# Kernel optimization log

Measured on AMD Instinct MI355X. Metric: run time of the kernel, lower is better.

Reference implementation:

```python
import jax, jax.numpy as jnp
import numpy as np

INS, OUTS = 768, 64
B, S = 8, 2048


def setup_inputs() -> dict:
    key = jax.random.key(0)
    ks = jax.random.split(key, 7)
    scale = 1.0 / np.sqrt(INS)
    inputs = jax.random.normal(ks[0], (B, S, INS), dtype=jnp.float32)
    Wq = jax.random.uniform(ks[1], (INS, OUTS), jnp.float32, -scale, scale)
    bq = jax.random.uniform(ks[2], (OUTS,), jnp.float32, -scale, scale)
    Wk = jax.random.uniform(ks[3], (INS, OUTS), jnp.float32, -scale, scale)
    bk = jax.random.uniform(ks[4], (OUTS,), jnp.float32, -scale, scale)
    Wv = jax.random.uniform(ks[5], (INS, OUTS), jnp.float32, -scale, scale)
    bv = jax.random.uniform(ks[6], (OUTS,), jnp.float32, -scale, scale)
    return {"inputs": inputs, "Wq": Wq, "bq": bq, "Wk": Wk, "bk": bk, "Wv": Wv, "bv": bv}


def reference(inputs, Wq, bq, Wk, bk, Wv, bv):
    # QKV projections: [B, S, ins] @ [ins, outs] -> [B, S, outs]
    q = jnp.einsum('bsi,io->bso', inputs, Wq) + bq
    k = jnp.einsum('bsi,io->bso', inputs, Wk) + bk
    v = jnp.einsum('bsi,io->bso', inputs, Wv) + bv
    dim_k = k.shape[-1]
    # scores: [B, S, S] (materialized, as in the original bmm-based impl)
    att = jnp.einsum('bqd,bkd->bqk', q, k) / jnp.sqrt(jnp.asarray(dim_k, q.dtype))
    att_soft = jax.nn.softmax(att, axis=-1)
    out = jnp.einsum('bqk,bkd->bqd', att_soft, v)
    return out
```

## Files before the change

### kernel.cpp

```cpp
#include <hip/hip_runtime.h>
#include <hip/hip_bf16.h>
#include <stdint.h>

#define INS 768
#define OUTS 64
#define BB 8
#define SS 2048
#define LDP 40

typedef __attribute__((ext_vector_type(8))) short short8;
typedef __attribute__((ext_vector_type(4))) float f32x4;

__device__ inline unsigned short f2bf(float f) {
  union { float f; uint32_t u; } v; v.f = f;
  uint32_t r = v.u + 0x7FFFu + ((v.u >> 16) & 1u);
  return (unsigned short)(r >> 16);
}

__device__ inline short8 cvt8hw(float4 a, float4 b) {
  union { __hip_bfloat162 h[4]; short8 s; } u;
  u.h[0] = __float22bfloat162_rn(make_float2(a.x, a.y));
  u.h[1] = __float22bfloat162_rn(make_float2(a.z, a.w));
  u.h[2] = __float22bfloat162_rn(make_float2(b.x, b.y));
  u.h[3] = __float22bfloat162_rn(make_float2(b.z, b.w));
  return u.s;
}
__device__ inline short8 cvt8w(const float* wf, float scl) {
  union { __hip_bfloat162 h[4]; short8 s; } u;
#pragma unroll
  for (int j = 0; j < 4; ++j)
    u.h[j] = __float22bfloat162_rn(make_float2(wf[2 * j] * scl, wf[2 * j + 1] * scl));
  return u.s;
}

__global__ __launch_bounds__(512) void qkv(
    const float* __restrict__ X,
    const float* __restrict__ Wq, const float* __restrict__ bq,
    const float* __restrict__ Wk, const float* __restrict__ bk,
    const float* __restrict__ Wv, const float* __restrict__ bv,
    unsigned short* __restrict__ Qg, unsigned short* __restrict__ Kg,
    unsigned short* __restrict__ Vtg) {
  __shared__ float Cbuf[4][64][13];
  const int tid  = threadIdx.x;
  const int wave = tid >> 6, lane = tid & 63;
  const int chg  = wave & 3, kh = wave >> 2;
  const int quad = lane >> 4, l16 = lane & 15;
  const int row0 = blockIdx.x * 16;
  const float* Xr = X + (size_t)(row0 + l16) * INS + kh * 384 + quad * 8;

  const float* Wm[3]; const float* Bm[3]; float scl[3]; int col0[3];
#pragma unroll
  for (int nt = 0; nt < 3; ++nt) {
    const int n0 = chg * 48 + nt * 16;
    const int mat = n0 >> 6;
    col0[nt] = n0 & 63;
    if (mat == 0)      { Wm[nt] = Wq; Bm[nt] = bq; scl[nt] = 0.125f; }
    else if (mat == 1) { Wm[nt] = Wk; Bm[nt] = bk; scl[nt] = 1.0f; }
    else               { Wm[nt] = Wv; Bm[nt] = bv; scl[nt] = 1.0f; }
  }

  f32x4 acc[3];
#pragma unroll
  for (int i = 0; i < 3; ++i) acc[i] = (f32x4){0.f, 0.f, 0.f, 0.f};

#pragma unroll 2
  for (int kc = 0; kc < 12; ++kc) {
    const int ko = kc * 32;
    const int kk = kh * 384 + ko;
    float4 x0 = *reinterpret_cast<const float4*>(Xr + ko);
    float4 x1 = *reinterpret_cast<const float4*>(Xr + ko + 4);
    float wf[3][8];
#pragma unroll
    for (int nt = 0; nt < 3; ++nt) {
      const float* src = Wm[nt] + (size_t)(kk + quad * 8) * OUTS + col0[nt] + l16;
#pragma unroll
      for (int j = 0; j < 8; ++j) wf[nt][j] = src[(size_t)j * OUTS];
    }
    short8 a = cvt8hw(x0, x1);
#pragma unroll
    for (int nt = 0; nt < 3; ++nt) {
      short8 b = cvt8w(wf[nt], scl[nt]);
      acc[nt] = __builtin_amdgcn_mfma_f32_16x16x32_bf16(a, b, acc[nt], 0, 0, 0);
    }
  }

  if (kh == 1) {
#pragma unroll
    for (int nt = 0; nt < 3; ++nt)
#pragma unroll
      for (int r = 0; r < 4; ++r) Cbuf[chg][lane][nt * 4 + r] = acc[nt][r];
  }
  __syncthreads();
  if (kh == 0) {
#pragma unroll
    for (int nt = 0; nt < 3; ++nt)
#pragma unroll
      for (int r = 0; r < 4; ++r) acc[nt][r] += Cbuf[chg][lane][nt * 4 + r];

    const int gm0 = row0 + quad * 4;
#pragma unroll
    for (int nt = 0; nt < 3; ++nt) {
      const int n = chg * 48 + nt * 16 + l16;
      const float bias = Bm[nt][col0[nt] + l16] * scl[nt];
      if (n < 128) {
        unsigned short* dstbase = (n < 64) ? Qg : Kg;
        const int nn = n & 63;
#pragma unroll
        for (int r = 0; r < 4; ++r)
          dstbase[(size_t)(gm0 + r) * OUTS + nn] = f2bf(acc[nt][r] + bias);
      } else {
        const int d = n - 128;
        const int batch = gm0 >> 11, s0 = gm0 & 2047;
        ushort4 pk;
        pk.x = f2bf(acc[nt][0] + bias);
        pk.y = f2bf(acc[nt][1] + bias);
        pk.z = f2bf(acc[nt][2] + bias);
        pk.w = f2bf(acc[nt][3] + bias);
        *reinterpret_cast<ushort4*>(&Vtg[((size_t)batch * OUTS + d) * SS + s0]) = pk;
      }
    }
  }
}

__global__ __launch_bounds__(256) void attn(
    const unsigned short* __restrict__ Qg, const unsigned short* __restrict__ Kg,
    const unsigned short* __restrict__ Vtg,
    float* __restrict__ OP, float* __restrict__ LS) {
  __shared__ __align__(16) unsigned short Ps[4][2][16 * LDP];
  const int tid  = threadIdx.x;
  const int wave = tid >> 6, lane = tid & 63;
  const int quad = lane >> 4, l16 = lane & 15;
  const int bt  = blockIdx.x >> 6;
  const int rem = blockIdx.x & 63;
  const int qb  = rem >> 2, ksl = rem & 3;
  const int q0 = qb * 128 + wave * 32;
  const unsigned short* Qb = Qg + (size_t)bt * SS * OUTS;
  const unsigned short* Kb = Kg + (size_t)bt * SS * OUTS;
  const unsigned short* Vb = Vtg + (size_t)bt * OUTS * SS;

  short8 aq[2][2];
#pragma unroll
  for (int mh = 0; mh < 2; ++mh)
#pragma unroll
    for (int ks = 0; ks < 2; ++ks)
      aq[mh][ks] = *reinterpret_cast<const short8*>(
          Qb + (size_t)(q0 + mh * 16 + l16) * OUTS + ks * 32 + quad * 8);

  f32x4 oacc[2][4];
#pragma unroll
  for (int mh = 0; mh < 2; ++mh)
#pragma unroll
    for (int nt = 0; nt < 4; ++nt) oacc[mh][nt] = (f32x4){0.f, 0.f, 0.f, 0.f};
  float lsum[2][4] = {{0.f,0.f,0.f,0.f},{0.f,0.f,0.f,0.f}};

  const int jbeg = ksl * 512;
  for (int j0 = jbeg; j0 < jbeg + 512; j0 += 32) {
    short8 bk[2][2], bv[4];
#pragma unroll
    for (int nt2 = 0; nt2 < 2; ++nt2)
#pragma unroll
      for (int ks = 0; ks < 2; ++ks)
        bk[nt2][ks] = *reinterpret_cast<const short8*>(
            Kb + (size_t)(j0 + nt2 * 16 + l16) * OUTS + ks * 32 + quad * 8);
#pragma unroll
    for (int nt = 0; nt < 4; ++nt)
      bv[nt] = *reinterpret_cast<const short8*>(
          Vb + (size_t)(nt * 16 + l16) * SS + j0 + quad * 8);

#pragma unroll
    for (int mh = 0; mh < 2; ++mh) {
      f32x4 sc[2];
      sc[0] = (f32x4){0.f,0.f,0.f,0.f}; sc[1] = (f32x4){0.f,0.f,0.f,0.f};
#pragma unroll
      for (int ks = 0; ks < 2; ++ks)
#pragma unroll
        for (int nt2 = 0; nt2 < 2; ++nt2)
          sc[nt2] = __builtin_amdgcn_mfma_f32_16x16x32_bf16(aq[mh][ks], bk[nt2][ks], sc[nt2], 0, 0, 0);

      unsigned short* Pw = Ps[wave][mh];
#pragma unroll
      for (int nt2 = 0; nt2 < 2; ++nt2)
#pragma unroll
        for (int r = 0; r < 4; ++r) {
          float p = __expf(sc[nt2][r]);
          lsum[mh][r] += p;
          Pw[(quad * 4 + r) * LDP + nt2 * 16 + l16] = f2bf(p);
        }
      short8 ap = *reinterpret_cast<const short8*>(&Pw[l16 * LDP + quad * 8]);
#pragma unroll
      for (int nt = 0; nt < 4; ++nt)
        oacc[mh][nt] = __builtin_amdgcn_mfma_f32_16x16x32_bf16(ap, bv[nt], oacc[mh][nt], 0, 0, 0);
    }
  }

#pragma unroll
  for (int st = 1; st < 16; st <<= 1)
#pragma unroll
    for (int mh = 0; mh < 2; ++mh)
#pragma unroll
      for (int r = 0; r < 4; ++r) lsum[mh][r] += __shfl_xor(lsum[mh][r], st, 64);

  float* OPb = OP + ((size_t)ksl * BB + bt) * SS * OUTS;
#pragma unroll
  for (int mh = 0; mh < 2; ++mh)
#pragma unroll
    for (int nt = 0; nt < 4; ++nt)
#pragma unroll
      for (int r = 0; r < 4; ++r) {
        int q = q0 + mh * 16 + quad * 4 + r;
        OPb[(size_t)q * OUTS + nt * 16 + l16] = oacc[mh][nt][r];
      }
  if (l16 == 0) {
#pragma unroll
    for (int mh = 0; mh < 2; ++mh)
#pragma unroll
      for (int r = 0; r < 4; ++r)
        LS[(size_t)ksl * BB * SS + bt * SS + q0 + mh * 16 + quad * 4 + r] = lsum[mh][r];
  }
}

__global__ __launch_bounds__(256) void combine(
    const float* __restrict__ OP, const float* __restrict__ LS,
    float* __restrict__ out) {
  const size_t i4 = (size_t)blockIdx.x * 256 + threadIdx.x;
  const size_t row = (i4 * 4) >> 6;
  float4 o = make_float4(0.f, 0.f, 0.f, 0.f);
  float l = 0.f;
#pragma unroll
  for (int ks = 0; ks < 4; ++ks) {
    float4 t = reinterpret_cast<const float4*>(OP + (size_t)ks * BB * SS * OUTS)[i4];
    o.x += t.x; o.y += t.y; o.z += t.z; o.w += t.w;
    l += LS[(size_t)ks * BB * SS + row];
  }
  const float inv = 1.0f / l;
  reinterpret_cast<float4*>(out)[i4] = make_float4(o.x * inv, o.y * inv, o.z * inv, o.w * inv);
}

extern "C" void kernel_launch(void* const* d_in, const int* in_sizes, int n_in,
                              void* d_out, int out_size, void* d_ws, size_t ws_size,
                              hipStream_t stream) {
  const float* X  = (const float*)d_in[0];
  const float* Wq = (const float*)d_in[1];
  const float* bq = (const float*)d_in[2];
  const float* Wk = (const float*)d_in[3];
  const float* bk = (const float*)d_in[4];
  const float* Wv = (const float*)d_in[5];
  const float* bv = (const float*)d_in[6];
  float* out = (float*)d_out;

  char* ws = (char*)d_ws;
  unsigned short* Qg  = (unsigned short*)(ws);
  unsigned short* Kg  = (unsigned short*)(ws + (size_t)2 * 1024 * 1024);
  unsigned short* Vtg = (unsigned short*)(ws + (size_t)4 * 1024 * 1024);
  float*          OP  = (float*)(ws + (size_t)7 * 1024 * 1024);
  float*          LS  = (float*)(ws + (size_t)23 * 1024 * 1024);

  qkv<<<1024, 512, 0, stream>>>(X, Wq, bq, Wk, bk, Wv, bv, Qg, Kg, Vtg);
  attn<<<512, 256, 0, stream>>>(Qg, Kg, Vtg, OP, LS);
  combine<<<1024, 256, 0, stream>>>(OP, LS, out);
}
```

Before: 171.3 us.

## Drop split-K attention and combine kernel; stage K/V tiles in shared memory

The attention kernel now walks all 2048 keys in one block per 64-query tile and normalises by the row sum before writing the final output directly. This removes the separate combine kernel and the large fp32 partial-output and row-sum buffers. K and transposed V tiles of 128 keys are loaded cooperatively into padded shared memory and shared by the four waves, replacing per-wave global loads. In exchange the grid halves to 256 blocks, so each CU holds fewer waves. The tile loop is single-buffered with two barriers per step, which may expose load latency.

After: 199.0 us. 16.2% more time.

```diff
diff --git a/kernel.cpp b/kernel.cpp
--- a/kernel.cpp
+++ b/kernel.cpp
@@ -6,7 +6,6 @@
 #define OUTS 64
 #define BB 8
 #define SS 2048
-#define LDP 40
 
 typedef __attribute__((ext_vector_type(8))) short short8;
 typedef __attribute__((ext_vector_type(4))) float f32x4;
@@ -122,118 +121,104 @@
   }
 }
 
+#define LDK 72
+#define LDV 136
+#define LDPR 136
+
 __global__ __launch_bounds__(256) void attn(
     const unsigned short* __restrict__ Qg, const unsigned short* __restrict__ Kg,
-    const unsigned short* __restrict__ Vtg,
-    float* __restrict__ OP, float* __restrict__ LS) {
-  __shared__ __align__(16) unsigned short Ps[4][2][16 * LDP];
+    const unsigned short* __restrict__ Vtg, float* __restrict__ out) {
+  __shared__ __align__(16) unsigned short Ks[128 * LDK];
+  __shared__ __align__(16) unsigned short Vts[64 * LDV];
+  __shared__ __align__(16) unsigned short Ps[4][16 * LDPR];
   const int tid  = threadIdx.x;
   const int wave = tid >> 6, lane = tid & 63;
   const int quad = lane >> 4, l16 = lane & 15;
-  const int bt  = blockIdx.x >> 6;
-  const int rem = blockIdx.x & 63;
-  const int qb  = rem >> 2, ksl = rem & 3;
-  const int q0 = qb * 128 + wave * 32;
+  const int bt = blockIdx.x >> 5, qt = blockIdx.x & 31;
+  const int q0 = qt * 64;
   const unsigned short* Qb = Qg + (size_t)bt * SS * OUTS;
   const unsigned short* Kb = Kg + (size_t)bt * SS * OUTS;
   const unsigned short* Vb = Vtg + (size_t)bt * OUTS * SS;
 
-  short8 aq[2][2];
-#pragma unroll
-  for (int mh = 0; mh < 2; ++mh)
-#pragma unroll
-    for (int ks = 0; ks < 2; ++ks)
-      aq[mh][ks] = *reinterpret_cast<const short8*>(
-          Qb + (size_t)(q0 + mh * 16 + l16) * OUTS + ks * 32 + quad * 8);
-
-  f32x4 oacc[2][4];
-#pragma unroll
-  for (int mh = 0; mh < 2; ++mh)
-#pragma unroll
-    for (int nt = 0; nt < 4; ++nt) oacc[mh][nt] = (f32x4){0.f, 0.f, 0.f, 0.f};
-  float lsum[2][4] = {{0.f,0.f,0.f,0.f},{0.f,0.f,0.f,0.f}};
-
-  const int jbeg = ksl * 512;
-  for (int j0 = jbeg; j0 < jbeg + 512; j0 += 32) {
-    short8 bk[2][2], bv[4];
-#pragma unroll
-    for (int nt2 = 0; nt2 < 2; ++nt2)
-#pragma unroll
-      for (int ks = 0; ks < 2; ++ks)
-        bk[nt2][ks] = *reinterpret_cast<const short8*>(
-            Kb + (size_t)(j0 + nt2 * 16 + l16) * OUTS + ks * 32 + quad * 8);
-#pragma unroll
-    for (int nt = 0; nt < 4; ++nt)
-      bv[nt] = *reinterpret_cast<const short8*>(
-          Vb + (size_t)(nt * 16 + l16) * SS + j0 + quad * 8);
-
-#pragma unroll
-    for (int mh = 0; mh < 2; ++mh) {
-      f32x4 sc[2];
-      sc[0] = (f32x4){0.f,0.f,0.f,0.f}; sc[1] = (f32x4){0.f,0.f,0.f,0.f};
-#pragma unroll
-      for (int ks = 0; ks < 2; ++ks)
-#pragma unroll
-        for (int nt2 = 0; nt2 < 2; ++nt2)
-          sc[nt2] = __builtin_amdgcn_mfma_f32_16x16x32_bf16(aq[mh][ks], bk[nt2][ks], sc[nt2], 0, 0, 0);
-
-      unsigned short* Pw = Ps[wave][mh];
-#pragma unroll
-      for (int nt2 = 0; nt2 < 2; ++nt2)
-#pragma unroll
-        for (int r = 0; r < 4; ++r) {
-          float p = __expf(sc[nt2][r]);
-          lsum[mh][r] += p;
-          Pw[(quad * 4 + r) * LDP + nt2 * 16 + l16] = f2bf(p);
-        }
-      short8 ap = *reinterpret_cast<const short8*>(&Pw[l16 * LDP + quad * 8]);
-#pragma unroll
-      for (int nt = 0; nt < 4; ++nt)
-        oacc[mh][nt] = __builtin_amdgcn_mfma_f32_16x16x32_bf16(ap, bv[nt], oacc[mh][nt], 0, 0, 0);
-    }
-  }
-
-#pragma unroll
-  for (int st = 1; st < 16; st <<= 1)
-#pragma unroll
-    for (int mh = 0; mh < 2; ++mh)
-#pragma unroll
-      for (int r = 0; r < 4; ++r) lsum[mh][r] += __shfl_xor(lsum[mh][r], st, 64);
-
-  float* OPb = OP + ((size_t)ksl * BB + bt) * SS * OUTS;
-#pragma unroll
-  for (int mh = 0; mh < 2; ++mh)
-#pragma unroll
-    for (int nt = 0; nt < 4; ++nt)
-#pragma unroll
-      for (int r = 0; r < 4; ++r) {
-        int q = q0 + mh * 16 + quad * 4 + r;
-        OPb[(size_t)q * OUTS + nt * 16 + l16] = oacc[mh][nt][r];
+  short8 aq[2];
+#pragma unroll
+  for (int ks = 0; ks < 2; ++ks)
+    aq[ks] = *reinterpret_cast<const short8*>(
+        Qb + (size_t)(q0 + wave * 16 + l16) * OUTS + ks * 32 + quad * 8);
+
+  f32x4 oacc[4];
+#pragma unroll
+  for (int i = 0; i < 4; ++i) oacc[i] = (f32x4){0.f, 0.f, 0.f, 0.f};
+  float lsum[4] = {0.f, 0.f, 0.f, 0.f};
+
+  for (int j0 = 0; j0 < SS; j0 += 128) {
+#pragma unroll
+    for (int rep = 0; rep < 4; ++rep) {
+      int c = tid + rep * 256;
+      int r = c >> 3, ch = c & 7;
+      *reinterpret_cast<int4*>(&Ks[r * LDK + ch * 8]) =
+          *reinterpret_cast<const int4*>(Kb + (size_t)(j0 + r) * OUTS + ch * 8);
+    }
+#pragma unroll
+    for (int rep = 0; rep < 4; ++rep) {
+      int c = tid + rep * 256;
+      int d = c >> 4, ch = c & 15;
+      *reinterpret_cast<int4*>(&Vts[d * LDV + ch * 8]) =
+          *reinterpret_cast<const int4*>(Vb + (size_t)d * SS + j0 + ch * 8);
+    }
+    __syncthreads();
+
+    f32x4 sc[8];
+#pragma unroll
+    for (int nt = 0; nt < 8; ++nt) sc[nt] = (f32x4){0.f, 0.f, 0.f, 0.f};
+#pragma unroll
+    for (int ks = 0; ks < 2; ++ks) {
+#pragma unroll
+      for (int nt = 0; nt < 8; ++nt) {
+        short8 b = *reinterpret_cast<const short8*>(&Ks[(nt * 16 + l16) * LDK + ks * 32 + quad * 8]);
+        sc[nt] = __builtin_amdgcn_mfma_f32_16x16x32_bf16(aq[ks], b, sc[nt], 0, 0, 0);
       }
-  if (l16 == 0) {
-#pragma unroll
-    for (int mh = 0; mh < 2; ++mh)
+    }
+
+    float p[8][4];
+    float rs[4] = {0.f, 0.f, 0.f, 0.f};
+#pragma unroll
+    for (int nt = 0; nt < 8; ++nt)
+#pragma unroll
+      for (int r = 0; r < 4; ++r) { p[nt][r] = __expf(sc[nt][r]); rs[r] += p[nt][r]; }
+#pragma unroll
+    for (int st = 1; st < 16; st <<= 1)
+#pragma unroll
+      for (int r = 0; r < 4; ++r) rs[r] += __shfl_xor(rs[r], st, 64);
+#pragma unroll
+    for (int r = 0; r < 4; ++r) lsum[r] += rs[r];
+
+    unsigned short* Pw = Ps[wave];
+#pragma unroll
+    for (int nt = 0; nt < 8; ++nt)
 #pragma unroll
       for (int r = 0; r < 4; ++r)
-        LS[(size_t)ksl * BB * SS + bt * SS + q0 + mh * 16 + quad * 4 + r] = lsum[mh][r];
-  }
-}
-
-__global__ __launch_bounds__(256) void combine(
-    const float* __restrict__ OP, const float* __restrict__ LS,
-    float* __restrict__ out) {
-  const size_t i4 = (size_t)blockIdx.x * 256 + threadIdx.x;
-  const size_t row = (i4 * 4) >> 6;
-  float4 o = make_float4(0.f, 0.f, 0.f, 0.f);
-  float l = 0.f;
-#pragma unroll
-  for (int ks = 0; ks < 4; ++ks) {
-    float4 t = reinterpret_cast<const float4*>(OP + (size_t)ks * BB * SS * OUTS)[i4];
-    o.x += t.x; o.y += t.y; o.z += t.z; o.w += t.w;
-    l += LS[(size_t)ks * BB * SS + row];
-  }
-  const float inv = 1.0f / l;
-  reinterpret_cast<float4*>(out)[i4] = make_float4(o.x * inv, o.y * inv, o.z * inv, o.w * inv);
+        Pw[(quad * 4 + r) * LDPR + nt * 16 + l16] = f2bf(p[nt][r]);
+
+#pragma unroll
+    for (int ks = 0; ks < 4; ++ks) {
+      short8 a = *reinterpret_cast<const short8*>(&Pw[l16 * LDPR + ks * 32 + quad * 8]);
+#pragma unroll
+      for (int nt = 0; nt < 4; ++nt) {
+        short8 b = *reinterpret_cast<const short8*>(&Vts[(nt * 16 + l16) * LDV + ks * 32 + quad * 8]);
+        oacc[nt] = __builtin_amdgcn_mfma_f32_16x16x32_bf16(a, b, oacc[nt], 0, 0, 0);
+      }
+    }
+    __syncthreads();
+  }
+
+#pragma unroll
+  for (int nt = 0; nt < 4; ++nt)
+#pragma unroll
+    for (int r = 0; r < 4; ++r) {
+      int q = q0 + wave * 16 + quad * 4 + r;
+      out[((size_t)bt * SS + q) * OUTS + nt * 16 + l16] = oacc[nt][r] / lsum[r];
+    }
 }
 
 extern "C" void kernel_launch(void* const* d_in, const int* in_sizes, int n_in,
@@ -252,10 +237,7 @@
   unsigned short* Qg  = (unsigned short*)(ws);
   unsigned short* Kg  = (unsigned short*)(ws + (size_t)2 * 1024 * 1024);
   unsigned short* Vtg = (unsigned short*)(ws + (size_t)4 * 1024 * 1024);
-  float*          OP  = (float*)(ws + (size_t)7 * 1024 * 1024);
-  float*          LS  = (float*)(ws + (size_t)23 * 1024 * 1024);
 
   qkv<<<1024, 512, 0, stream>>>(X, Wq, bq, Wk, bk, Wv, bv, Qg, Kg, Vtg);
-  attn<<<512, 256, 0, stream>>>(Qg, Kg, Vtg, OP, LS);
-  combine<<<1024, 256, 0, stream>>>(OP, LS, out);
-}
+  attn<<<256, 256, 0, stream>>>(Qg, Kg, Vtg, out);
+}
```

## Fuse split-K combine into attention kernel via in-block LDS reduction

Applied to the files above, without the earlier changes.

The attention kernel now gives each block 16 query rows, with its four waves each covering a quarter of the key range. Partial outputs and row sums are reduced through shared memory and written straight to the output, so the separate combine kernel and its 16 MB fp32 partial-buffer round trip go away. K/V fragment loads are also double-buffered in registers so the next tile's loads overlap the current tile's compute. In exchange, each wave now reuses each K/V fragment for only 16 query rows instead of 32, which roughly doubles K/V global/L2 traffic, and it needs more LDS per block.

After: 190.7 us. 1.11x slower.

```diff
diff --git a/kernel.cpp b/kernel.cpp
--- a/kernel.cpp
+++ b/kernel.cpp
@@ -122,118 +122,111 @@
   }
 }
 
+struct AttF { short8 k[2][2]; short8 v[4]; };
+
 __global__ __launch_bounds__(256) void attn(
     const unsigned short* __restrict__ Qg, const unsigned short* __restrict__ Kg,
-    const unsigned short* __restrict__ Vtg,
-    float* __restrict__ OP, float* __restrict__ LS) {
-  __shared__ __align__(16) unsigned short Ps[4][2][16 * LDP];
+    const unsigned short* __restrict__ Vtg, float* __restrict__ out) {
+  __shared__ __align__(16) char smem[21760];
   const int tid  = threadIdx.x;
+  const int blk  = blockIdx.x;
   const int wave = tid >> 6, lane = tid & 63;
   const int quad = lane >> 4, l16 = lane & 15;
-  const int bt  = blockIdx.x >> 6;
-  const int rem = blockIdx.x & 63;
-  const int qb  = rem >> 2, ksl = rem & 3;
-  const int q0 = qb * 128 + wave * 32;
+
+  float* Obuf = reinterpret_cast<float*>(smem);
+  float* Lbuf = reinterpret_cast<float*>(smem + 16384);
+  unsigned short* Ps = reinterpret_cast<unsigned short*>(smem + 16640);
+  const int bt = blk >> 7;
+  const int q0 = (blk & 127) * 16;
   const unsigned short* Qb = Qg + (size_t)bt * SS * OUTS;
   const unsigned short* Kb = Kg + (size_t)bt * SS * OUTS;
   const unsigned short* Vb = Vtg + (size_t)bt * OUTS * SS;
-
-  short8 aq[2][2];
-#pragma unroll
-  for (int mh = 0; mh < 2; ++mh)
+  const int jbeg = wave * 512;
+  unsigned short* Pw = Ps + wave * 16 * LDP;
+
+  short8 aq[2];
+#pragma unroll
+  for (int ks = 0; ks < 2; ++ks)
+    aq[ks] = *reinterpret_cast<const short8*>(
+        Qb + (size_t)(q0 + l16) * OUTS + ks * 32 + quad * 8);
+
+  f32x4 oacc[4];
+#pragma unroll
+  for (int nt = 0; nt < 4; ++nt) oacc[nt] = (f32x4){0.f, 0.f, 0.f, 0.f};
+  float lsum[4] = {0.f, 0.f, 0.f, 0.f};
+
+  auto load = [&](int it, AttF& f) {
+    const int j0 = jbeg + it * 32;
+#pragma unroll
+    for (int nt2 = 0; nt2 < 2; ++nt2)
+#pragma unroll
+      for (int ks = 0; ks < 2; ++ks)
+        f.k[nt2][ks] = *reinterpret_cast<const short8*>(
+            Kb + (size_t)(j0 + nt2 * 16 + l16) * OUTS + ks * 32 + quad * 8);
+#pragma unroll
+    for (int nt = 0; nt < 4; ++nt)
+      f.v[nt] = *reinterpret_cast<const short8*>(
+          Vb + (size_t)(nt * 16 + l16) * SS + j0 + quad * 8);
+  };
+  auto comp = [&](AttF& f) {
+    f32x4 sc[2];
+    sc[0] = (f32x4){0.f,0.f,0.f,0.f}; sc[1] = (f32x4){0.f,0.f,0.f,0.f};
 #pragma unroll
     for (int ks = 0; ks < 2; ++ks)
-      aq[mh][ks] = *reinterpret_cast<const short8*>(
-          Qb + (size_t)(q0 + mh * 16 + l16) * OUTS + ks * 32 + quad * 8);
-
-  f32x4 oacc[2][4];
-#pragma unroll
-  for (int mh = 0; mh < 2; ++mh)
-#pragma unroll
-    for (int nt = 0; nt < 4; ++nt) oacc[mh][nt] = (f32x4){0.f, 0.f, 0.f, 0.f};
-  float lsum[2][4] = {{0.f,0.f,0.f,0.f},{0.f,0.f,0.f,0.f}};
-
-  const int jbeg = ksl * 512;
-  for (int j0 = jbeg; j0 < jbeg + 512; j0 += 32) {
-    short8 bk[2][2], bv[4];
+#pragma unroll
+      for (int nt2 = 0; nt2 < 2; ++nt2)
+        sc[nt2] = __builtin_amdgcn_mfma_f32_16x16x32_bf16(aq[ks], f.k[nt2][ks], sc[nt2], 0, 0, 0);
 #pragma unroll
     for (int nt2 = 0; nt2 < 2; ++nt2)
 #pragma unroll
-      for (int ks = 0; ks < 2; ++ks)
-        bk[nt2][ks] = *reinterpret_cast<const short8*>(
-            Kb + (size_t)(j0 + nt2 * 16 + l16) * OUTS + ks * 32 + quad * 8);
+      for (int r = 0; r < 4; ++r) {
+        float p = __expf(sc[nt2][r]);
+        lsum[r] += p;
+        Pw[(quad * 4 + r) * LDP + nt2 * 16 + l16] = f2bf(p);
+      }
+    short8 ap = *reinterpret_cast<const short8*>(&Pw[l16 * LDP + quad * 8]);
 #pragma unroll
     for (int nt = 0; nt < 4; ++nt)
-      bv[nt] = *reinterpret_cast<const short8*>(
-          Vb + (size_t)(nt * 16 + l16) * SS + j0 + quad * 8);
-
-#pragma unroll
-    for (int mh = 0; mh < 2; ++mh) {
-      f32x4 sc[2];
-      sc[0] = (f32x4){0.f,0.f,0.f,0.f}; sc[1] = (f32x4){0.f,0.f,0.f,0.f};
-#pragma unroll
-      for (int ks = 0; ks < 2; ++ks)
-#pragma unroll
-        for (int nt2 = 0; nt2 < 2; ++nt2)
-          sc[nt2] = __builtin_amdgcn_mfma_f32_16x16x32_bf16(aq[mh][ks], bk[nt2][ks], sc[nt2], 0, 0, 0);
-
-      unsigned short* Pw = Ps[wave][mh];
-#pragma unroll
-      for (int nt2 = 0; nt2 < 2; ++nt2)
-#pragma unroll
-        for (int r = 0; r < 4; ++r) {
-          float p = __expf(sc[nt2][r]);
-          lsum[mh][r] += p;
-          Pw[(quad * 4 + r) * LDP + nt2 * 16 + l16] = f2bf(p);
-        }
-      short8 ap = *reinterpret_cast<const short8*>(&Pw[l16 * LDP + quad * 8]);
-#pragma unroll
-      for (int nt = 0; nt < 4; ++nt)
-        oacc[mh][nt] = __builtin_amdgcn_mfma_f32_16x16x32_bf16(ap, bv[nt], oacc[mh][nt], 0, 0, 0);
-    }
+      oacc[nt] = __builtin_amdgcn_mfma_f32_16x16x32_bf16(ap, f.v[nt], oacc[nt], 0, 0, 0);
+  };
+
+  AttF fa, fb;
+  load(0, fa);
+  for (int it = 0; it < 16; it += 2) {
+    load(it + 1, fb);
+    comp(fa);
+    if (it + 2 < 16) load(it + 2, fa);
+    comp(fb);
   }
 
 #pragma unroll
   for (int st = 1; st < 16; st <<= 1)
 #pragma unroll
-    for (int mh = 0; mh < 2; ++mh)
-#pragma unroll
-      for (int r = 0; r < 4; ++r) lsum[mh][r] += __shfl_xor(lsum[mh][r], st, 64);
-
-  float* OPb = OP + ((size_t)ksl * BB + bt) * SS * OUTS;
-#pragma unroll
-  for (int mh = 0; mh < 2; ++mh)
-#pragma unroll
-    for (int nt = 0; nt < 4; ++nt)
-#pragma unroll
-      for (int r = 0; r < 4; ++r) {
-        int q = q0 + mh * 16 + quad * 4 + r;
-        OPb[(size_t)q * OUTS + nt * 16 + l16] = oacc[mh][nt][r];
-      }
+    for (int r = 0; r < 4; ++r) lsum[r] += __shfl_xor(lsum[r], st, 64);
+
+#pragma unroll
+  for (int nt = 0; nt < 4; ++nt)
+#pragma unroll
+    for (int r = 0; r < 4; ++r)
+      Obuf[(wave * 16 + quad * 4 + r) * 64 + nt * 16 + l16] = oacc[nt][r];
   if (l16 == 0) {
 #pragma unroll
-    for (int mh = 0; mh < 2; ++mh)
-#pragma unroll
-      for (int r = 0; r < 4; ++r)
-        LS[(size_t)ksl * BB * SS + bt * SS + q0 + mh * 16 + quad * 4 + r] = lsum[mh][r];
-  }
-}
-
-__global__ __launch_bounds__(256) void combine(
-    const float* __restrict__ OP, const float* __restrict__ LS,
-    float* __restrict__ out) {
-  const size_t i4 = (size_t)blockIdx.x * 256 + threadIdx.x;
-  const size_t row = (i4 * 4) >> 6;
-  float4 o = make_float4(0.f, 0.f, 0.f, 0.f);
+    for (int r = 0; r < 4; ++r) Lbuf[wave * 16 + quad * 4 + r] = lsum[r];
+  }
+  __syncthreads();
+
+  const int row = tid >> 4, c = (tid & 15) * 4;
+  float4 s = make_float4(0.f, 0.f, 0.f, 0.f);
   float l = 0.f;
 #pragma unroll
-  for (int ks = 0; ks < 4; ++ks) {
-    float4 t = reinterpret_cast<const float4*>(OP + (size_t)ks * BB * SS * OUTS)[i4];
-    o.x += t.x; o.y += t.y; o.z += t.z; o.w += t.w;
-    l += LS[(size_t)ks * BB * SS + row];
+  for (int w = 0; w < 4; ++w) {
+    float4 t = *reinterpret_cast<const float4*>(&Obuf[((w * 16 + row) * 64) + c]);
+    s.x += t.x; s.y += t.y; s.z += t.z; s.w += t.w;
+    l += Lbuf[w * 16 + row];
   }
   const float inv = 1.0f / l;
-  reinterpret_cast<float4*>(out)[i4] = make_float4(o.x * inv, o.y * inv, o.z * inv, o.w * inv);
+  *reinterpret_cast<float4*>(&out[((size_t)(bt * SS + q0 + row)) * OUTS + c]) =
+      make_float4(s.x * inv, s.y * inv, s.z * inv, s.w * inv);
 }
 
 extern "C" void kernel_launch(void* const* d_in, const int* in_sizes, int n_in,
@@ -252,10 +245,7 @@
   unsigned short* Qg  = (unsigned short*)(ws);
   unsigned short* Kg  = (unsigned short*)(ws + (size_t)2 * 1024 * 1024);
   unsigned short* Vtg = (unsigned short*)(ws + (size_t)4 * 1024 * 1024);
-  float*          OP  = (float*)(ws + (size_t)7 * 1024 * 1024);
-  float*          LS  = (float*)(ws + (size_t)23 * 1024 * 1024);
 
   qkv<<<1024, 512, 0, stream>>>(X, Wq, bq, Wk, bk, Wv, bv, Qg, Kg, Vtg);
-  attn<<<512, 256, 0, stream>>>(Qg, Kg, Vtg, OP, LS);
-  combine<<<1024, 256, 0, stream>>>(OP, LS, out);
-}
+  attn<<<1024, 256, 0, stream>>>(Qg, Kg, Vtg, out);
+}
```
